# Performance work log

Hardware: AMD Instinct MI355X
Metric: run time of the kernel (lower is better)

## Reference

```python
import jax, jax.numpy as jnp
import numpy as np

BLOCK = 32          # QLinearLPBQ block_size
W_BITS = 4          # low-precision blockwise weight quantization
ACT_BITS = 16       # ActivationQDQ(bits=16)


def act_qdq(x):
    # per-tensor symmetric 16-bit fake quant-dequant (dynamic absmax scale)
    qmax = 2.0 ** (ACT_BITS - 1) - 1.0  # 32767
    scale = jnp.maximum(jnp.max(jnp.abs(x)) / qmax, 1e-12)
    return jnp.clip(jnp.round(x / scale), -qmax - 1.0, qmax) * scale


def fixed_qdq_u16(x):
    # FixedActivationQDQ: scale = 1/65536, zero_point = 0, unsigned 16-bit grid
    scale = 1.0 / 65536.0
    return jnp.clip(jnp.round(x / scale), 0.0, 65535.0) * scale


def lpbq_dequant(w):
    # blockwise (per output row, per 32-wide input block) 4-bit fake quant-dequant
    O, I = w.shape
    qmax = 2.0 ** (W_BITS - 1) - 1.0  # 7
    wb = w.reshape(O, I // BLOCK, BLOCK)
    s = jnp.maximum(jnp.max(jnp.abs(wb), axis=-1, keepdims=True) / qmax, 1e-12)
    wq = jnp.clip(jnp.round(wb / s), -qmax - 1.0, qmax) * s
    return wq.reshape(O, I)


def setup_inputs() -> dict:
    key = jax.random.key(0)
    k1, k2, k3, k4 = jax.random.split(key, 4)
    B, S, H, I = 2, 4096, 1024, 3072
    x = jax.random.normal(k1, (B, S, H), jnp.float32)
    w_gate = jax.random.normal(k2, (I, H), jnp.float32) * 0.02
    w_up = jax.random.normal(k3, (I, H), jnp.float32) * 0.02
    w_down = jax.random.normal(k4, (H, I), jnp.float32) * 0.02
    return {"x": x, "w_gate": w_gate, "w_up": w_up, "w_down": w_down}


def reference(x, w_gate, w_up, w_down):
    # x: [B, S, H]
    x = act_qdq(x)                                        # up_proj_input_qdq
    up = act_qdq(x @ lpbq_dequant(w_up).T)                # up_proj + output qdq -> [B,S,I]
    gate = act_qdq(x @ lpbq_dequant(w_gate).T)            # gate_proj + output qdq
    sig = fixed_qdq_u16(jax.nn.sigmoid(gate))             # sigmoid on fixed u16 grid
    gate = act_qdq(gate * sig)                            # SiLU (x*sigmoid) + qdq
    o = act_qdq(gate * up)                                # down_proj_input_qdq
    return o @ lpbq_dequant(w_down).T                     # [B, S, H]
```

## Files before the change

kernel.cpp:

```cpp
#include <hip/hip_runtime.h>
#include <hip/hip_bf16.h>
#include <stdint.h>


#define M_ROWS 8192
#define H_DIM 1024
#define I_DIM 3072

typedef unsigned short u16;
typedef unsigned int u32;
typedef __attribute__((ext_vector_type(8))) short bf16x8;
typedef __attribute__((ext_vector_type(4))) float f32x4;

__device__ __forceinline__ float bf2f(u16 v) { return __uint_as_float(((u32)v) << 16); }
__device__ __forceinline__ u16 f2bf(float f) {
  u32 u = __float_as_uint(f);
  u32 r = (u + 0x7fffu + ((u >> 16) & 1u)) >> 16;
  return (u16)r;
}
__device__ __forceinline__ float qdq16i(float x, float inv, float s) {
  float q = rintf(x * inv);
  q = fminf(fmaxf(q, -32768.f), 32767.f);
  return q * s;
}

__device__ __forceinline__ float scale_read(const u32* __restrict__ scal, int s) {
  u32 m = 0;
#pragma unroll
  for (int j = 0; j < 16; ++j) m = max(m, scal[j * 16 + s]);
  return fmaxf(__uint_as_float(m) / 32767.f, 1e-12f);
}

__device__ __forceinline__ void load_lds16(const u16* g, u16* lds) {
  __builtin_amdgcn_global_load_lds(
      (const __attribute__((address_space(1))) u32*)g,
      (__attribute__((address_space(3))) u32*)lds, 16, 0, 0);
}

__device__ __forceinline__ void block_amax_atomic(float mx, u32* scal, int s) {
#pragma unroll
  for (int off = 32; off; off >>= 1) mx = fmaxf(mx, __shfl_xor(mx, off));
  __shared__ float red[4];
  const int lane = threadIdx.x & 63, wave = threadIdx.x >> 6;
  if (lane == 0) red[wave] = mx;
  __syncthreads();
  if (threadIdx.x == 0) {
    float m = fmaxf(fmaxf(red[0], red[1]), fmaxf(red[2], red[3]));
    atomicMax(scal + (blockIdx.x & 15) * 16 + s, __float_as_uint(m));
  }
}

template <int K>
__device__ __forceinline__ void gemm_core(const u16* __restrict__ Ablk,
                                          const u16* __restrict__ Bblk,
                                          f32x4 acc[4][4]) {
  __shared__ __align__(16) u16 As[128 * 32];
  __shared__ __align__(16) u16 Bs[128 * 32];
  const int tid = threadIdx.x;
  const int lane = tid & 63, wave = tid >> 6;
  const int wm = wave >> 1, wn = wave & 1;
  const int quad = lane >> 4, mrow = lane & 15;

  const int c0 = tid, c1 = tid + 256;
  const int r0 = c0 >> 2, g0 = ((c0 & 3) ^ (r0 & 3)) * 8;
  const int r1 = c1 >> 2, g1 = ((c1 & 3) ^ (r1 & 3)) * 8;
  const u16* a0 = Ablk + (size_t)r0 * K + g0;
  const u16* a1 = Ablk + (size_t)r1 * K + g1;
  const u16* b0 = Bblk + (size_t)r0 * K + g0;
  const u16* b1 = Bblk + (size_t)r1 * K + g1;
  u16* lA0 = &As[c0 * 8];
  u16* lA1 = &As[c1 * 8];
  u16* lB0 = &Bs[c0 * 8];
  u16* lB1 = &Bs[c1 * 8];

  int aoff[4], boff[4];
  const int lq = (quad ^ (mrow & 3)) * 8;
#pragma unroll
  for (int t = 0; t < 4; ++t) {
    aoff[t] = (wm * 64 + t * 16 + mrow) * 32 + lq;
    boff[t] = (wn * 64 + t * 16 + mrow) * 32 + lq;
  }

  for (int k0 = 0; k0 < K; k0 += 32) {
    __syncthreads();
    load_lds16(a0 + k0, lA0);
    load_lds16(a1 + k0, lA1);
    load_lds16(b0 + k0, lB0);
    load_lds16(b1 + k0, lB1);
    __syncthreads();
    bf16x8 af[4], bfr[4];
#pragma unroll
    for (int t = 0; t < 4; ++t) {
      af[t] = *(const bf16x8*)&As[aoff[t]];
      bfr[t] = *(const bf16x8*)&Bs[boff[t]];
    }
#pragma unroll
    for (int i = 0; i < 4; ++i)
#pragma unroll
      for (int j = 0; j < 4; ++j)
        acc[i][j] = __builtin_amdgcn_mfma_f32_16x16x32_bf16(af[i], bfr[j], acc[i][j], 0, 0, 0);
  }
}

__global__ void __launch_bounds__(256) kgemm1(const u16* __restrict__ xq,
                                              const u16* __restrict__ wcat,
                                              u16* __restrict__ up, u16* __restrict__ gh,
                                              u32* __restrict__ scal) {
  const int tileN = blockIdx.x * 128;
  const int tileM = blockIdx.y * 128;
  f32x4 acc[4][4];
#pragma unroll
  for (int i = 0; i < 4; ++i)
#pragma unroll
    for (int j = 0; j < 4; ++j) acc[i][j] = (f32x4){0.f, 0.f, 0.f, 0.f};
  gemm_core<H_DIM>(xq + (size_t)tileM * H_DIM, wcat + (size_t)tileN * H_DIM, acc);

  u16* outp;
  int ncol, slot;
  if (tileN < I_DIM) { outp = up; ncol = tileN; slot = 1; }
  else               { outp = gh; ncol = tileN - I_DIM; slot = 2; }

  const int lane = threadIdx.x & 63, wave = threadIdx.x >> 6;
  const int wm = wave >> 1, wn = wave & 1;
  const int rb = (lane >> 4) * 4, cb = lane & 15;
  float mx = 0.f;
#pragma unroll
  for (int i = 0; i < 4; ++i) {
#pragma unroll
    for (int j = 0; j < 4; ++j) {
      size_t base = (size_t)(tileM + wm * 64 + i * 16 + rb) * I_DIM +
                    (size_t)(ncol + wn * 64 + j * 16 + cb);
#pragma unroll
      for (int r = 0; r < 4; ++r) {
        float v = acc[i][j][r];
        mx = fmaxf(mx, fabsf(v));
        outp[base + (size_t)r * I_DIM] = f2bf(v);
      }
    }
  }
  block_amax_atomic(mx, scal, slot);
}

__global__ void __launch_bounds__(256) kgemm2(const u16* __restrict__ oq,
                                              const u16* __restrict__ wdq,
                                              float* __restrict__ out) {
  const int tileN = blockIdx.x * 128;
  const int tileM = blockIdx.y * 128;
  f32x4 acc[4][4];
#pragma unroll
  for (int i = 0; i < 4; ++i)
#pragma unroll
    for (int j = 0; j < 4; ++j) acc[i][j] = (f32x4){0.f, 0.f, 0.f, 0.f};
  gemm_core<I_DIM>(oq + (size_t)tileM * I_DIM, wdq + (size_t)tileN * I_DIM, acc);

  const int lane = threadIdx.x & 63, wave = threadIdx.x >> 6;
  const int wm = wave >> 1, wn = wave & 1;
  const int rb = (lane >> 4) * 4, cb = lane & 15;
#pragma unroll
  for (int i = 0; i < 4; ++i) {
#pragma unroll
    for (int j = 0; j < 4; ++j) {
      size_t base = (size_t)(tileM + wm * 64 + i * 16 + rb) * H_DIM +
                    (size_t)(tileN + wn * 64 + j * 16 + cb);
#pragma unroll
      for (int r = 0; r < 4; ++r) out[base + (size_t)r * H_DIM] = acc[i][j][r];
    }
  }
}

__global__ void __launch_bounds__(256) kabsmax(const float4* __restrict__ x, int n4,
                                               u32* __restrict__ scal) {
  float mx = 0.f;
  for (int i = blockIdx.x * blockDim.x + threadIdx.x; i < n4; i += gridDim.x * blockDim.x) {
    float4 v = x[i];
    mx = fmaxf(fmaxf(fabsf(v.x), fabsf(v.y)), fmaxf(fmaxf(fabsf(v.z), fabsf(v.w)), mx));
  }
  block_amax_atomic(mx, scal, 0);
}

__global__ void __launch_bounds__(256) kdequant(const float* __restrict__ wu,
                                                const float* __restrict__ wg,
                                                const float* __restrict__ wdn,
                                                u16* __restrict__ wcat, u16* __restrict__ wdq) {
  const int gid = blockIdx.x * 256 + threadIdx.x;
  const int unit = gid >> 3, l8 = gid & 7;
  const float* src;
  u16* dst;
  int u;
  if (unit < 98304)       { src = wu;  dst = wcat;            u = unit; }
  else if (unit < 196608) { src = wg;  dst = wcat + 3145728;  u = unit - 98304; }
  else                    { src = wdn; dst = wdq;             u = unit - 196608; }
  const size_t off = (size_t)u * 32 + (size_t)l8 * 4;
  float4 v = *(const float4*)(src + off);
  float m = fmaxf(fmaxf(fabsf(v.x), fabsf(v.y)), fmaxf(fabsf(v.z), fabsf(v.w)));
  m = fmaxf(m, __shfl_xor(m, 1));
  m = fmaxf(m, __shfl_xor(m, 2));
  m = fmaxf(m, __shfl_xor(m, 4));
  const float s = fmaxf(m / 7.0f, 1e-12f);
  const float inv = 1.0f / s;
  float vv[4] = {v.x, v.y, v.z, v.w};
  u16 o[4];
#pragma unroll
  for (int e = 0; e < 4; ++e) {
    float q = rintf(vv[e] * inv);
    q = fminf(fmaxf(q, -8.f), 7.f);
    o[e] = f2bf(q * s);
  }
  *(ushort4*)(dst + off) = make_ushort4(o[0], o[1], o[2], o[3]);
}

__global__ void __launch_bounds__(256) kqdqx(const float4* __restrict__ x,
                                             ushort4* __restrict__ xq,
                                             const u32* __restrict__ scal) {
  const float s = scale_read(scal, 0);
  const float inv = 1.0f / s;
  const int i = blockIdx.x * 256 + threadIdx.x;
  float4 v = x[i];
  ushort4 o;
  o.x = f2bf(qdq16i(v.x, inv, s));
  o.y = f2bf(qdq16i(v.y, inv, s));
  o.z = f2bf(qdq16i(v.z, inv, s));
  o.w = f2bf(qdq16i(v.w, inv, s));
  xq[i] = o;
}

#define GH4 ((M_ROWS * I_DIM) / 8)
#define EW_BLOCKS 2048

__global__ void __launch_bounds__(256) kswiglu(uint4* __restrict__ gh, u32* __restrict__ scal) {
  const float sg = scale_read(scal, 2);
  const float inv = 1.0f / sg;
  float mx = 0.f;
  for (int i = blockIdx.x * 256 + threadIdx.x; i < GH4; i += EW_BLOCKS * 256) {
    union { uint4 v; u16 us[8]; } u;
    u.v = gh[i];
#pragma unroll
    for (int e = 0; e < 8; ++e) {
      float g = qdq16i(bf2f(u.us[e]), inv, sg);
      float sig = __builtin_amdgcn_rcpf(1.f + __expf(-g));
      float sq = fminf(fmaxf(rintf(sig * 65536.f), 0.f), 65535.f) * (1.f / 65536.f);
      float h = g * sq;
      mx = fmaxf(mx, fabsf(h));
      u.us[e] = f2bf(h);
    }
    gh[i] = u.v;
  }
  block_amax_atomic(mx, scal, 3);
}

__global__ void __launch_bounds__(256) kmulo(uint4* __restrict__ gh, const uint4* __restrict__ up,
                                             u32* __restrict__ scal) {
  const float sh = scale_read(scal, 3);
  const float su = scale_read(scal, 1);
  const float ih = 1.0f / sh, iu = 1.0f / su;
  float mx = 0.f;
  for (int i = blockIdx.x * 256 + threadIdx.x; i < GH4; i += EW_BLOCKS * 256) {
    union { uint4 v; u16 us[8]; } a, b;
    a.v = gh[i];
    b.v = up[i];
#pragma unroll
    for (int e = 0; e < 8; ++e) {
      float o = qdq16i(bf2f(a.us[e]), ih, sh) * qdq16i(bf2f(b.us[e]), iu, su);
      mx = fmaxf(mx, fabsf(o));
      a.us[e] = f2bf(o);
    }
    gh[i] = a.v;
  }
  block_amax_atomic(mx, scal, 4);
}

__global__ void __launch_bounds__(256) kqdqo(uint4* __restrict__ gh, const u32* __restrict__ scal) {
  const float so = scale_read(scal, 4);
  const float inv = 1.0f / so;
  const int i = blockIdx.x * 256 + threadIdx.x;
  union { uint4 v; u16 us[8]; } u;
  u.v = gh[i];
#pragma unroll
  for (int e = 0; e < 8; ++e) u.us[e] = f2bf(qdq16i(bf2f(u.us[e]), inv, so));
  gh[i] = u.v;
}

extern "C" void kernel_launch(void* const* d_in, const int* in_sizes, int n_in,
                              void* d_out, int out_size, void* d_ws, size_t ws_size,
                              hipStream_t stream) {
  (void)in_sizes; (void)n_in; (void)out_size; (void)ws_size;
  const float* x   = (const float*)d_in[0];
  const float* wg  = (const float*)d_in[1];
  const float* wu  = (const float*)d_in[2];
  const float* wdn = (const float*)d_in[3];
  float* out = (float*)d_out;
  char* ws = (char*)d_ws;

  u32* scal = (u32*)ws;
  u16* xq   = (u16*)(ws + 1024);
  u16* wcat = xq + (size_t)M_ROWS * H_DIM;
  u16* wdq  = wcat + (size_t)2 * I_DIM * H_DIM;
  u16* up   = wdq + (size_t)H_DIM * I_DIM;
  u16* gh   = up + (size_t)M_ROWS * I_DIM;

  hipMemsetAsync(scal, 0, 1024, stream);
  kabsmax<<<1024, 256, 0, stream>>>((const float4*)x, (M_ROWS * H_DIM) / 4, scal);
  kdequant<<<9216, 256, 0, stream>>>(wu, wg, wdn, wcat, wdq);
  kqdqx<<<(M_ROWS * H_DIM) / 4 / 256, 256, 0, stream>>>((const float4*)x, (ushort4*)xq, scal);
  kgemm1<<<dim3(48, 64), 256, 0, stream>>>(xq, wcat, up, gh, scal);
  kswiglu<<<EW_BLOCKS, 256, 0, stream>>>((uint4*)gh, scal);
  kmulo<<<EW_BLOCKS, 256, 0, stream>>>((uint4*)gh, (const uint4*)up, scal);
  kqdqo<<<(M_ROWS * I_DIM) / 8 / 256, 256, 0, stream>>>((uint4*)gh, scal);
  kgemm2<<<dim3(8, 64), 256, 0, stream>>>(gh, wdq, out);
}
```

Before: 376.0 us.

## Stage GEMM1 epilogue through LDS and recompute SiLU to drop an intermediate write

The GEMM1 epilogue now packs each bf16 output sub-tile into shared memory per wave and writes rows with 16-byte vector stores instead of scattered 2-byte stores. The LDS swizzle changes to XOR with (row>>1)&3 to alter bank mapping. The SwiGLU pass becomes read-only, computing only the absmax, and the multiply kernel recomputes the sigmoid-gated value from the gate. This removes a full write of the gate-sized intermediate at the cost of repeating the exp and rcp work and adding extra syncs in the epilogue.

```diff
diff --git a/kernel.cpp b/kernel.cpp
--- a/kernel.cpp
+++ b/kernel.cpp
@@ -53,17 +53,17 @@
 template <int K>
 __device__ __forceinline__ void gemm_core(const u16* __restrict__ Ablk,
                                           const u16* __restrict__ Bblk,
-                                          f32x4 acc[4][4]) {
-  __shared__ __align__(16) u16 As[128 * 32];
-  __shared__ __align__(16) u16 Bs[128 * 32];
+                                          f32x4 acc[4][4], u16* smem) {
+  u16* As = smem;
+  u16* Bs = smem + 4096;
   const int tid = threadIdx.x;
   const int lane = tid & 63, wave = tid >> 6;
   const int wm = wave >> 1, wn = wave & 1;
   const int quad = lane >> 4, mrow = lane & 15;
 
   const int c0 = tid, c1 = tid + 256;
-  const int r0 = c0 >> 2, g0 = ((c0 & 3) ^ (r0 & 3)) * 8;
-  const int r1 = c1 >> 2, g1 = ((c1 & 3) ^ (r1 & 3)) * 8;
+  const int r0 = c0 >> 2, g0 = ((c0 & 3) ^ ((r0 >> 1) & 3)) * 8;
+  const int r1 = c1 >> 2, g1 = ((c1 & 3) ^ ((r1 >> 1) & 3)) * 8;
   const u16* a0 = Ablk + (size_t)r0 * K + g0;
   const u16* a1 = Ablk + (size_t)r1 * K + g1;
   const u16* b0 = Bblk + (size_t)r0 * K + g0;
@@ -74,7 +74,7 @@
   u16* lB1 = &Bs[c1 * 8];
 
   int aoff[4], boff[4];
-  const int lq = (quad ^ (mrow & 3)) * 8;
+  const int lq = (quad ^ ((mrow >> 1) & 3)) * 8;
 #pragma unroll
   for (int t = 0; t < 4; ++t) {
     aoff[t] = (wm * 64 + t * 16 + mrow) * 32 + lq;
@@ -106,6 +106,7 @@
                                               const u16* __restrict__ wcat,
                                               u16* __restrict__ up, u16* __restrict__ gh,
                                               u32* __restrict__ scal) {
+  __shared__ __align__(16) u16 smem[8192];
   const int tileN = blockIdx.x * 128;
   const int tileM = blockIdx.y * 128;
   f32x4 acc[4][4];
@@ -113,7 +114,7 @@
   for (int i = 0; i < 4; ++i)
 #pragma unroll
     for (int j = 0; j < 4; ++j) acc[i][j] = (f32x4){0.f, 0.f, 0.f, 0.f};
-  gemm_core<H_DIM>(xq + (size_t)tileM * H_DIM, wcat + (size_t)tileN * H_DIM, acc);
+  gemm_core<H_DIM>(xq + (size_t)tileM * H_DIM, wcat + (size_t)tileN * H_DIM, acc, smem);
 
   u16* outp;
   int ncol, slot;
@@ -123,20 +124,27 @@
   const int lane = threadIdx.x & 63, wave = threadIdx.x >> 6;
   const int wm = wave >> 1, wn = wave & 1;
   const int rb = (lane >> 4) * 4, cb = lane & 15;
+  const int erow = lane >> 2, echk = lane & 3;
+  u16* wbase = smem + wave * 1152;
+  const u16* rbase = smem + wave * 1152 + erow * 72;
   float mx = 0.f;
 #pragma unroll
   for (int i = 0; i < 4; ++i) {
-#pragma unroll
-    for (int j = 0; j < 4; ++j) {
-      size_t base = (size_t)(tileM + wm * 64 + i * 16 + rb) * I_DIM +
-                    (size_t)(ncol + wn * 64 + j * 16 + cb);
+    __syncthreads();
+#pragma unroll
+    for (int j = 0; j < 4; ++j)
 #pragma unroll
       for (int r = 0; r < 4; ++r) {
         float v = acc[i][j][r];
         mx = fmaxf(mx, fabsf(v));
-        outp[base + (size_t)r * I_DIM] = f2bf(v);
+        wbase[(rb + r) * 72 + j * 16 + cb] = f2bf(v);
       }
-    }
+    __syncthreads();
+    uint4 v0 = *(const uint4*)(rbase + echk * 8);
+    uint4 v1 = *(const uint4*)(rbase + (echk + 4) * 8);
+    size_t grow = (size_t)(tileM + wm * 64 + i * 16 + erow) * I_DIM + (ncol + wn * 64);
+    *(uint4*)(outp + grow + echk * 8) = v0;
+    *(uint4*)(outp + grow + (echk + 4) * 8) = v1;
   }
   block_amax_atomic(mx, scal, slot);
 }
@@ -144,6 +152,7 @@
 __global__ void __launch_bounds__(256) kgemm2(const u16* __restrict__ oq,
                                               const u16* __restrict__ wdq,
                                               float* __restrict__ out) {
+  __shared__ __align__(16) u16 smem[8192];
   const int tileN = blockIdx.x * 128;
   const int tileM = blockIdx.y * 128;
   f32x4 acc[4][4];
@@ -151,7 +160,7 @@
   for (int i = 0; i < 4; ++i)
 #pragma unroll
     for (int j = 0; j < 4; ++j) acc[i][j] = (f32x4){0.f, 0.f, 0.f, 0.f};
-  gemm_core<I_DIM>(oq + (size_t)tileM * I_DIM, wdq + (size_t)tileN * I_DIM, acc);
+  gemm_core<I_DIM>(oq + (size_t)tileM * I_DIM, wdq + (size_t)tileN * I_DIM, acc, smem);
 
   const int lane = threadIdx.x & 63, wave = threadIdx.x >> 6;
   const int wm = wave >> 1, wn = wave & 1;
@@ -227,7 +236,8 @@
 #define GH4 ((M_ROWS * I_DIM) / 8)
 #define EW_BLOCKS 2048
 
-__global__ void __launch_bounds__(256) kswiglu(uint4* __restrict__ gh, u32* __restrict__ scal) {
+__global__ void __launch_bounds__(256) kswiglu(const uint4* __restrict__ gh,
+                                               u32* __restrict__ scal) {
   const float sg = scale_read(scal, 2);
   const float inv = 1.0f / sg;
   float mx = 0.f;
@@ -239,20 +249,18 @@
       float g = qdq16i(bf2f(u.us[e]), inv, sg);
       float sig = __builtin_amdgcn_rcpf(1.f + __expf(-g));
       float sq = fminf(fmaxf(rintf(sig * 65536.f), 0.f), 65535.f) * (1.f / 65536.f);
-      float h = g * sq;
-      mx = fmaxf(mx, fabsf(h));
-      u.us[e] = f2bf(h);
+      mx = fmaxf(mx, fabsf(g * sq));
     }
-    gh[i] = u.v;
   }
   block_amax_atomic(mx, scal, 3);
 }
 
 __global__ void __launch_bounds__(256) kmulo(uint4* __restrict__ gh, const uint4* __restrict__ up,
                                              u32* __restrict__ scal) {
+  const float sg = scale_read(scal, 2);
   const float sh = scale_read(scal, 3);
   const float su = scale_read(scal, 1);
-  const float ih = 1.0f / sh, iu = 1.0f / su;
+  const float ig = 1.0f / sg, ih = 1.0f / sh, iu = 1.0f / su;
   float mx = 0.f;
   for (int i = blockIdx.x * 256 + threadIdx.x; i < GH4; i += EW_BLOCKS * 256) {
     union { uint4 v; u16 us[8]; } a, b;
@@ -260,7 +268,11 @@
     b.v = up[i];
 #pragma unroll
     for (int e = 0; e < 8; ++e) {
-      float o = qdq16i(bf2f(a.us[e]), ih, sh) * qdq16i(bf2f(b.us[e]), iu, su);
+      float g = qdq16i(bf2f(a.us[e]), ig, sg);
+      float sig = __builtin_amdgcn_rcpf(1.f + __expf(-g));
+      float sq = fminf(fmaxf(rintf(sig * 65536.f), 0.f), 65535.f) * (1.f / 65536.f);
+      u16 hb = f2bf(g * sq);
+      float o = qdq16i(bf2f(hb), ih, sh) * qdq16i(bf2f(b.us[e]), iu, su);
       mx = fmaxf(mx, fabsf(o));
       a.us[e] = f2bf(o);
     }
@@ -303,7 +315,7 @@
   kdequant<<<9216, 256, 0, stream>>>(wu, wg, wdn, wcat, wdq);
   kqdqx<<<(M_ROWS * H_DIM) / 4 / 256, 256, 0, stream>>>((const float4*)x, (ushort4*)xq, scal);
   kgemm1<<<dim3(48, 64), 256, 0, stream>>>(xq, wcat, up, gh, scal);
-  kswiglu<<<EW_BLOCKS, 256, 0, stream>>>((uint4*)gh, scal);
+  kswiglu<<<EW_BLOCKS, 256, 0, stream>>>((const uint4*)gh, scal);
   kmulo<<<EW_BLOCKS, 256, 0, stream>>>((uint4*)gh, (const uint4*)up, scal);
   kqdqo<<<(M_ROWS * I_DIM) / 8 / 256, 256, 0, stream>>>((uint4*)gh, scal);
   kgemm2<<<dim3(8, 64), 256, 0, stream>>>(gh, wdq, out);
```

Result: no change. 375.1 us (-0.2%).
